# Performance work log

Measured on AMD Instinct MI355X. Metric: run time of the kernel, lower is better.

Reference implementation:

```python
import jax, jax.numpy as jnp
import numpy as np

NUM_HEADS = 4
NUM_GROUPS = 8
EPS = 1e-5


def setup_inputs() -> dict:
    key = jax.random.key(0)
    ks = jax.random.split(key, 4)
    b, c, h, w = 16, 512, 32, 32
    x = jax.random.normal(ks[0], (b, c, h, w), dtype=jnp.float32)
    norm_gamma = jnp.ones((c,), dtype=jnp.float32)
    norm_beta = jnp.zeros((c,), dtype=jnp.float32)
    qkv_w = jax.random.normal(ks[1], (3 * c, c), dtype=jnp.float32) * (c ** -0.5)
    qkv_b = jnp.zeros((3 * c,), dtype=jnp.float32)
    proj_w = jax.random.normal(ks[2], (c, c), dtype=jnp.float32) * (c ** -0.5)
    proj_b = jnp.zeros((c,), dtype=jnp.float32)
    return {"x": x, "norm_gamma": norm_gamma, "norm_beta": norm_beta,
            "qkv_w": qkv_w, "qkv_b": qkv_b, "proj_w": proj_w, "proj_b": proj_b}


def reference(x, norm_gamma, norm_beta, qkv_w, qkv_b, proj_w, proj_b):
    b, c, h, w = x.shape
    nh = NUM_HEADS
    dh = c // nh
    n = h * w
    # GroupNorm(8, c): normalize over (c/G, h, w) within each group, biased var
    xg = x.reshape(b, NUM_GROUPS, -1)
    mu = jnp.mean(xg, axis=-1, keepdims=True)
    var = jnp.var(xg, axis=-1, keepdims=True)
    xn = ((xg - mu) * jax.lax.rsqrt(var + EPS)).reshape(b, c, h, w)
    xn = xn * norm_gamma[:, None, None] + norm_beta[:, None, None]
    # QKV 1x1 conv == channel matmul
    qkv = jnp.einsum('oc,bchw->bohw', qkv_w, xn) + qkv_b[:, None, None]
    q, k, v = jnp.split(qkv, 3, axis=1)  # each [b, c, h, w]

    def to_heads(t):  # [b, c, h, w] -> [b, nh, n, dh]
        return t.reshape(b, nh, dh, n).transpose(0, 1, 3, 2)

    q, k, v = to_heads(q), to_heads(k), to_heads(v)
    scale = dh ** -0.5
    attn = jax.nn.softmax(jnp.einsum('bhnd,bhmd->bhnm', q, k) * scale, axis=-1)
    out = jnp.einsum('bhnm,bhmd->bhnd', attn, v)  # [b, nh, n, dh]
    out = out.transpose(0, 1, 3, 2).reshape(b, c, h, w)
    out = jnp.einsum('oc,bchw->bohw', proj_w, out) + proj_b[:, None, None]
    return x + out
```

## Files before the change

kernel.cpp:

```cpp
#include <hip/hip_runtime.h>

typedef unsigned short u16;
typedef unsigned int   u32;

typedef __attribute__((ext_vector_type(8)))  short bf16x8;
typedef __attribute__((ext_vector_type(16))) float f32x16;
#define MFMA32(a, b, c) __builtin_amdgcn_mfma_f32_32x32x16_bf16(a, b, c, 0, 0, 0)

__device__ __forceinline__ float bf2f(u16 h) { return __uint_as_float(((u32)h) << 16); }
__device__ __forceinline__ u16 f2bf(float f) {
  u32 u = __float_as_uint(f);
  u += 0x7fffu + ((u >> 16) & 1u);
  return (u16)(u >> 16);
}
__device__ __forceinline__ void unpack8(uint4 u, float* f) {
  f[0] = __uint_as_float(u.x << 16); f[1] = __uint_as_float(u.x & 0xffff0000u);
  f[2] = __uint_as_float(u.y << 16); f[3] = __uint_as_float(u.y & 0xffff0000u);
  f[4] = __uint_as_float(u.z << 16); f[5] = __uint_as_float(u.z & 0xffff0000u);
  f[6] = __uint_as_float(u.w << 16); f[7] = __uint_as_float(u.w & 0xffff0000u);
}
__device__ __forceinline__ void unpack4(uint2 u, float* f) {
  f[0] = __uint_as_float(u.x << 16); f[1] = __uint_as_float(u.x & 0xffff0000u);
  f[2] = __uint_as_float(u.y << 16); f[3] = __uint_as_float(u.y & 0xffff0000u);
}

template <bool F>
__device__ __forceinline__ void load8(const void* p, size_t idx, float* f) {
  if constexpr (F) {
    const float4* q = (const float4*)((const float*)p + idx);
    float4 a = q[0], b = q[1];
    f[0] = a.x; f[1] = a.y; f[2] = a.z; f[3] = a.w;
    f[4] = b.x; f[5] = b.y; f[6] = b.z; f[7] = b.w;
  } else {
    unpack8(*(const uint4*)((const u16*)p + idx), f);
  }
}
template <bool F>
__device__ __forceinline__ void load4(const void* p, size_t idx, float* f) {
  if constexpr (F) {
    float4 a = *(const float4*)((const float*)p + idx);
    f[0] = a.x; f[1] = a.y; f[2] = a.z; f[3] = a.w;
  } else {
    unpack4(*(const uint2*)((const u16*)p + idx), f);
  }
}
template <bool F>
__device__ __forceinline__ float load1(const void* p, size_t idx) {
  if constexpr (F) return ((const float*)p)[idx];
  else return bf2f(((const u16*)p)[idx]);
}

__device__ __forceinline__ void gl2lds16(const void* g, void* l) {
  __builtin_amdgcn_global_load_lds(
      (const __attribute__((address_space(1))) void*)g,
      (__attribute__((address_space(3))) void*)l, 16, 0, 0);
}

__global__ void detect_dtype(const void* __restrict__ x, int* __restrict__ flag) {
  if (threadIdx.x == 0 && blockIdx.x == 0) {
    const u32* p = (const u32*)x;
    int sane = 0;
    for (int i = 0; i < 256; ++i) {
      u32 e = (p[i] >> 7) & 0xFFu;
      sane += (e >= 100u && e <= 150u) ? 1 : 0;
    }
    *flag = (sane < 192) ? 1 : 0;
  }
}

__global__ void signal_ws(u16* __restrict__ out, int n) {
  int i = blockIdx.x * 256 + threadIdx.x;
  if (i < n) out[i] = 0x42C8;
}

#define SM_SCALE 0.08838834764831843f
#define QSC 0.12751743f


template <bool F>
__global__ void __launch_bounds__(256) wconv(const void* __restrict__ qkvw,
                                             const void* __restrict__ qkvb,
                                             u16* __restrict__ dst,
                                             const int* __restrict__ flag) {
  if ((flag[0] != 0) != F) return;
  int i = blockIdx.x * 256 + threadIdx.x;
  if (i < 786432) {
    dst[i] = F ? f2bf(((const float*)qkvw)[i]) : ((const u16*)qkvw)[i];
  } else if (i < 787968) {
    int j = i - 786432;
    dst[i] = F ? f2bf(((const float*)qkvb)[j]) : ((const u16*)qkvb)[j];
  }
}

template <bool F>
__global__ void __launch_bounds__(256) gn_norm(const void* __restrict__ x,
                                               const void* __restrict__ gamma,
                                               const void* __restrict__ beta,
                                               u16* __restrict__ xT,
                                               const int* __restrict__ flag) {
  if ((flag[0] != 0) != F) return;
  const int g = blockIdx.x, b = blockIdx.y;
  const int tid = threadIdx.x;
  const size_t base = (size_t)(b * 512 + g * 64) * 1024;
  float sum = 0.f, sq = 0.f;
  for (int i = tid; i < 8192; i += 256) {
    float f[8]; load8<F>(x, base + (size_t)i * 8, f);
#pragma unroll
    for (int m = 0; m < 8; ++m) { sum += f[m]; sq += f[m] * f[m]; }
  }
  __shared__ float ssum[256], ssq[256];
  ssum[tid] = sum; ssq[tid] = sq; __syncthreads();
  for (int off = 128; off > 0; off >>= 1) {
    if (tid < off) { ssum[tid] += ssum[tid + off]; ssq[tid] += ssq[tid + off]; }
    __syncthreads();
  }
  __shared__ float scb[64], bsb[64];
  if (tid < 64) {
    float mu  = ssum[0] * (1.f / 65536.f);
    float var = ssq[0] * (1.f / 65536.f) - mu * mu;
    float s = load1<F>(gamma, g * 64 + tid) * rsqrtf(var + 1e-5f);
    scb[tid] = s;
    bsb[tid] = load1<F>(beta, g * 64 + tid) - mu * s;
  }
  __syncthreads();

  __shared__ float Tf[64][65];
  for (int s0 = 0; s0 < 1024; s0 += 64) {
#pragma unroll
    for (int half = 0; half < 2; ++half) {
      int idx = tid + half * 256;
      int c_loc = idx >> 3, s8 = (idx & 7) * 8;
      float f[8];
      load8<F>(x, base + (size_t)c_loc * 1024 + s0 + s8, f);
      float sm = scb[c_loc], ba = bsb[c_loc];
#pragma unroll
      for (int m = 0; m < 8; ++m) Tf[s8 + m][c_loc] = f[m] * sm + ba;
    }
    __syncthreads();
#pragma unroll
    for (int half = 0; half < 2; ++half) {
      int idx = tid + half * 256;
      int s_loc = idx >> 3, c8 = (idx & 7) * 8;
      u32 pk[4];
#pragma unroll
      for (int m = 0; m < 4; ++m)
        pk[m] = (u32)f2bf(Tf[s_loc][c8 + 2 * m]) |
                ((u32)f2bf(Tf[s_loc][c8 + 2 * m + 1]) << 16);
      *(uint4*)(xT + (size_t)(b * 1024 + s0 + s_loc) * 512 + g * 64 + c8) =
          make_uint4(pk[0], pk[1], pk[2], pk[3]);
    }
    __syncthreads();
  }
}

template <bool QSCALE, bool BIASN>
__global__ void __launch_bounds__(256, 4)
gemm_lds(const u16* __restrict__ A, const u16* __restrict__ B,
         const u16* __restrict__ bias, u16* __restrict__ outp,
         size_t aOff, size_t aBatch, size_t bBatch, int biasOff, size_t oBatch) {
  const int n0 = blockIdx.x * 128;
  const int m0 = blockIdx.y * 128;
  const int b  = blockIdx.z;
  __shared__ __align__(16) u16 At[8192];
  __shared__ __align__(16) u16 Bt[8192];
  const int tid = threadIdx.x;
  const int w = tid >> 6, lane = tid & 63;
  const int lo = lane & 31, hi = lane >> 5;
  const int wm = w >> 1, wn = w & 1;
  const u16* Ab = A + aOff + (size_t)b * aBatch;
  const u16* Bb = B + (size_t)b * bBatch;
  const int srow = lane >> 3, spc = lane & 7;

  f32x16 cA[2][2];
#pragma unroll
  for (int i = 0; i < 2; ++i)
#pragma unroll
    for (int j = 0; j < 2; ++j)
#pragma unroll
      for (int r = 0; r < 16; ++r) cA[i][j][r] = 0.f;

  for (int kt = 0; kt < 8; ++kt) {
    const int kb = kt * 64;
#pragma unroll
    for (int c = 0; c < 4; ++c) {
      int grp = w * 4 + c;
      int row = grp * 8 + srow;
      int lc  = spc ^ (row & 7);
      gl2lds16(Ab + (size_t)(m0 + row) * 512 + kb + lc * 8, &At[grp * 512]);
      gl2lds16(Bb + (size_t)(n0 + row) * 512 + kb + lc * 8, &Bt[grp * 512]);
    }
    __syncthreads();
#pragma unroll
    for (int k16 = 0; k16 < 4; ++k16) {
      const int lc = k16 * 2 + hi;
      const int rA0 = wm * 64 + lo,  rA1 = rA0 + 32;
      const int rB0 = wn * 64 + lo,  rB1 = rB0 + 32;
      bf16x8 a0 = *(const bf16x8*)&At[rA0 * 64 + ((lc ^ (rA0 & 7)) << 3)];
      bf16x8 a1 = *(const bf16x8*)&At[rA1 * 64 + ((lc ^ (rA1 & 7)) << 3)];
      bf16x8 b0 = *(const bf16x8*)&Bt[rB0 * 64 + ((lc ^ (rB0 & 7)) << 3)];
      bf16x8 b1 = *(const bf16x8*)&Bt[rB1 * 64 + ((lc ^ (rB1 & 7)) << 3)];
      cA[0][0] = MFMA32(a0, b0, cA[0][0]);
      cA[0][1] = MFMA32(a0, b1, cA[0][1]);
      cA[1][0] = MFMA32(a1, b0, cA[1][0]);
      cA[1][1] = MFMA32(a1, b1, cA[1][1]);
    }
    __syncthreads();
  }

  float bcol[2];
  if constexpr (BIASN) {
    bcol[0] = bf2f(bias[biasOff + n0 + wn * 64 + lo]);
    bcol[1] = bf2f(bias[biasOff + n0 + wn * 64 + 32 + lo]);
  }
#pragma unroll
  for (int mt = 0; mt < 2; ++mt)
#pragma unroll
    for (int nt = 0; nt < 2; ++nt) {
      const int nbase = n0 + wn * 64 + nt * 32;
      float scl = 1.f;
      if constexpr (QSCALE) scl = (nbase < 512) ? QSC : 1.f;
#pragma unroll
      for (int r = 0; r < 16; ++r) {
        int m = m0 + wm * 64 + mt * 32 + (r & 3) + 8 * (r >> 2) + 4 * hi;
        int n = nbase + lo;
        float v = cA[mt][nt][r];
        if constexpr (BIASN) v += bcol[nt];
        else                 v += bf2f(bias[biasOff + m]);
        if constexpr (QSCALE) v *= scl;
        outp[(size_t)b * oBatch + (size_t)m * 1024 + n] = f2bf(v);
      }
    }
}

template <bool F, bool AEXT, bool BEXT, bool BIASN, bool RESID, bool FOUT>
__global__ void __launch_bounds__(256, 4)
gemm_mfma(const void* __restrict__ A, const void* __restrict__ B,
          const void* __restrict__ bias, const void* __restrict__ resid,
          void* __restrict__ outp,
          size_t aOff, size_t bOff, int biasOff,
          size_t aBatch, size_t bBatch, size_t oBatch, size_t rBatch,
          const int* __restrict__ flag) {
  if ((flag[0] != 0) != F) return;
  const int n0 = blockIdx.x * 128;
  const int m0 = blockIdx.y * 128;
  const int b  = blockIdx.z;
  __shared__ __align__(16) u16 At[128][72];
  __shared__ __align__(16) u16 Bt[128][72];
  const int tid = threadIdx.x;
  const int w = tid >> 6, lane = tid & 63;
  const int lo = lane & 31, hi = lane >> 5;
  const int wm = w >> 1, wn = w & 1;
  const size_t aBase = aOff + (size_t)b * aBatch;
  const size_t bBase = bOff + (size_t)b * bBatch;

  f32x16 cA[2][2];
#pragma unroll
  for (int i = 0; i < 2; ++i)
#pragma unroll
    for (int j = 0; j < 2; ++j)
#pragma unroll
      for (int r = 0; r < 16; ++r) cA[i][j][r] = 0.f;

  for (int kt = 0; kt < 8; ++kt) {
#pragma unroll
    for (int i = 0; i < 4; ++i) {
      int idx = tid + i * 256;
      int row = idx >> 3, kc = (idx & 7) * 8;
      int k = kt * 64 + kc;
      {
        if constexpr (AEXT && F) {
          float f[8]; load8<true>(A, aBase + (size_t)(m0 + row) * 512 + k, f);
          u32 w0 = (u32)f2bf(f[0]) | ((u32)f2bf(f[1]) << 16);
          u32 w1 = (u32)f2bf(f[2]) | ((u32)f2bf(f[3]) << 16);
          u32 w2 = (u32)f2bf(f[4]) | ((u32)f2bf(f[5]) << 16);
          u32 w3 = (u32)f2bf(f[6]) | ((u32)f2bf(f[7]) << 16);
          *(uint4*)&At[row][kc] = make_uint4(w0, w1, w2, w3);
        } else {
          *(uint4*)&At[row][kc] =
              *(const uint4*)((const u16*)A + aBase + (size_t)(m0 + row) * 512 + k);
        }
      }
      {
        if constexpr (BEXT && F) {
          float f[8]; load8<true>(B, bBase + (size_t)(n0 + row) * 512 + k, f);
          u32 w0 = (u32)f2bf(f[0]) | ((u32)f2bf(f[1]) << 16);
          u32 w1 = (u32)f2bf(f[2]) | ((u32)f2bf(f[3]) << 16);
          u32 w2 = (u32)f2bf(f[4]) | ((u32)f2bf(f[5]) << 16);
          u32 w3 = (u32)f2bf(f[6]) | ((u32)f2bf(f[7]) << 16);
          *(uint4*)&Bt[row][kc] = make_uint4(w0, w1, w2, w3);
        } else {
          *(uint4*)&Bt[row][kc] =
              *(const uint4*)((const u16*)B + bBase + (size_t)(n0 + row) * 512 + k);
        }
      }
    }
    __syncthreads();
#pragma unroll
    for (int k16 = 0; k16 < 4; ++k16) {
      const int ko = k16 * 16 + hi * 8;
      bf16x8 a0 = *(const bf16x8*)&At[wm * 64 + lo][ko];
      bf16x8 a1 = *(const bf16x8*)&At[wm * 64 + 32 + lo][ko];
      bf16x8 b0 = *(const bf16x8*)&Bt[wn * 64 + lo][ko];
      bf16x8 b1 = *(const bf16x8*)&Bt[wn * 64 + 32 + lo][ko];
      cA[0][0] = MFMA32(a0, b0, cA[0][0]);
      cA[0][1] = MFMA32(a0, b1, cA[0][1]);
      cA[1][0] = MFMA32(a1, b0, cA[1][0]);
      cA[1][1] = MFMA32(a1, b1, cA[1][1]);
    }
    __syncthreads();
  }

  float bcol[2];
  if constexpr (BIASN) {
    bcol[0] = load1<F>(bias, biasOff + n0 + wn * 64 + lo);
    bcol[1] = load1<F>(bias, biasOff + n0 + wn * 64 + 32 + lo);
  }
#pragma unroll
  for (int mt = 0; mt < 2; ++mt)
#pragma unroll
    for (int nt = 0; nt < 2; ++nt) {
#pragma unroll
      for (int r = 0; r < 16; ++r) {
        int m = m0 + wm * 64 + mt * 32 + (r & 3) + 8 * (r >> 2) + 4 * hi;
        int n = n0 + wn * 64 + nt * 32 + lo;
        float v = cA[mt][nt][r];
        if constexpr (BIASN) v += bcol[nt];
        else                 v += load1<F>(bias, biasOff + m);
        if constexpr (RESID)
          v += load1<F>(resid, (size_t)b * rBatch + (size_t)m * 1024 + n);
        size_t off = (size_t)b * oBatch + (size_t)m * 1024 + n;
        if constexpr (FOUT) ((float*)outp)[off] = v;
        else                ((u16*)outp)[off] = f2bf(v);
      }
    }
}

__global__ void __launch_bounds__(256, 2) attn4(const u16* __restrict__ qkT,
                                                const u16* __restrict__ V,
                                                u16* __restrict__ aout) {
  const int bh = blockIdx.x;
  const int q0 = blockIdx.y * 128;
  const int b = bh >> 2, h = bh & 3;
  const u16* qt = qkT + (size_t)b * 1048576;
  const u16* vb = V + (size_t)b * 524288 + (size_t)(h * 128) * 1024;
  __shared__ __align__(16) u16 smem[25600];
  const int tid = threadIdx.x;
  const int w = tid >> 6, lane = tid & 63;
  const int lo = lane & 31, hi = lane >> 5;

#pragma unroll
  for (int c = 0; c < 8; ++c) {
    int grp = w * 8 + c;
    int row = grp * 4 + (lane >> 4);
    int lc  = (lane & 15) ^ (row & 7);
    gl2lds16(qt + (size_t)(q0 + row) * 1024 + h * 128 + lc * 8, &smem[grp * 512]);
  }
  __syncthreads();
  bf16x8 qf[8];
  {
    const int row = 32 * w + lo;
#pragma unroll
    for (int k16 = 0; k16 < 8; ++k16) {
      int lc = k16 * 2 + hi;
      qf[k16] = *(const bf16x8*)&smem[row * 128 + ((lc ^ (row & 7)) << 3)];
    }
  }

  f32x16 o0, o1, o2, o3;
  float lp[16];
#pragma unroll
  for (int r = 0; r < 16; ++r) { o0[r] = 0.f; o1[r] = 0.f; o2[r] = 0.f; o3[r] = 0.f; lp[r] = 0.f; }

  for (int kt = 0; kt < 16; ++kt) {
    const int k0 = kt * 64;
    __syncthreads();
#pragma unroll
    for (int c = 0; c < 4; ++c) {
      int grp = w * 4 + c;
      {
        int row = grp * 4 + (lane >> 4);
        int lc  = (lane & 15) ^ (row & 7);
        gl2lds16(qt + (size_t)(k0 + row) * 1024 + 512 + h * 128 + lc * 8,
                 &smem[grp * 512]);
      }
      {
        int row = grp * 8 + (lane >> 3);
        int lc  = (lane & 7) ^ (row & 7);
        gl2lds16(vb + (size_t)row * 1024 + k0 + lc * 8, &smem[8192 + grp * 512]);
      }
    }
    __syncthreads();

    f32x16 s0, s1;
#pragma unroll
    for (int r = 0; r < 16; ++r) { s0[r] = 0.f; s1[r] = 0.f; }
#pragma unroll
    for (int k16 = 0; k16 < 8; ++k16) {
      const int lc = k16 * 2 + hi;
      const int r0 = lo, r1 = lo + 32;
      bf16x8 b0 = *(const bf16x8*)&smem[r0 * 128 + ((lc ^ (r0 & 7)) << 3)];
      bf16x8 b1 = *(const bf16x8*)&smem[r1 * 128 + ((lc ^ (r1 & 7)) << 3)];
      s0 = MFMA32(qf[k16], b0, s0);
      s1 = MFMA32(qf[k16], b1, s1);
    }

#pragma unroll
    for (int r = 0; r < 16; ++r) {
      float p0 = exp2f(s0[r]);
      float p1 = exp2f(s1[r]);
      lp[r] += p0 + p1;
      int row = (r & 3) + 8 * (r >> 2) + 4 * hi;
      smem[16384 + w * 2304 + row * 72 + lo]      = f2bf(p0);
      smem[16384 + w * 2304 + row * 72 + lo + 32] = f2bf(p1);
    }

#pragma unroll
    for (int k16v = 0; k16v < 4; ++k16v) {
      bf16x8 pa = *(const bf16x8*)&smem[16384 + w * 2304 + lo * 72 + k16v * 16 + hi * 8];
      const int lc = k16v * 2 + hi;
#pragma unroll
      for (int dt = 0; dt < 4; ++dt) {
        const int row = dt * 32 + lo;
        bf16x8 bv = *(const bf16x8*)&smem[8192 + row * 64 + ((lc ^ (row & 7)) << 3)];
        if (dt == 0) o0 = MFMA32(pa, bv, o0);
        else if (dt == 1) o1 = MFMA32(pa, bv, o1);
        else if (dt == 2) o2 = MFMA32(pa, bv, o2);
        else o3 = MFMA32(pa, bv, o3);
      }
    }
  }

#pragma unroll
  for (int r = 0; r < 16; ++r) {
    float su = lp[r];
    su += __shfl_xor(su, 1);  su += __shfl_xor(su, 2);
    su += __shfl_xor(su, 4);  su += __shfl_xor(su, 8);
    su += __shfl_xor(su, 16);
    float linv = 1.f / su;
    int q = q0 + 32 * w + (r & 3) + 8 * (r >> 2) + 4 * hi;
    size_t base = (size_t)(b * 1024 + q) * 512 + h * 128;
    aout[base +  0 + lo] = f2bf(o0[r] * linv);
    aout[base + 32 + lo] = f2bf(o1[r] * linv);
    aout[base + 64 + lo] = f2bf(o2[r] * linv);
    aout[base + 96 + lo] = f2bf(o3[r] * linv);
  }
}


template <bool F>
__global__ void __launch_bounds__(256) gn_stats(const void* __restrict__ x,
                                                const void* __restrict__ gamma,
                                                const void* __restrict__ beta,
                                                float* __restrict__ sc,
                                                float* __restrict__ bs,
                                                const int* __restrict__ flag) {
  if ((flag[0] != 0) != F) return;
  const int g = blockIdx.x, b = blockIdx.y;
  const int tid = threadIdx.x;
  const size_t base = (size_t)(b * 512 + g * 64) * 1024;
  float sum = 0.f, sq = 0.f;
  for (int i = tid; i < 8192; i += 256) {
    float f[8]; load8<F>(x, base + (size_t)i * 8, f);
#pragma unroll
    for (int m = 0; m < 8; ++m) { sum += f[m]; sq += f[m] * f[m]; }
  }
  __shared__ float ssum[256], ssq[256];
  ssum[tid] = sum; ssq[tid] = sq; __syncthreads();
  for (int off = 128; off > 0; off >>= 1) {
    if (tid < off) { ssum[tid] += ssum[tid + off]; ssq[tid] += ssq[tid + off]; }
    __syncthreads();
  }
  if (tid < 64) {
    float mu  = ssum[0] * (1.f / 65536.f);
    float var = ssq[0] * (1.f / 65536.f) - mu * mu;
    int c = g * 64 + tid;
    float s = load1<F>(gamma, c) * rsqrtf(var + 1e-5f);
    sc[b * 512 + c] = s;
    bs[b * 512 + c] = load1<F>(beta, c) - mu * s;
  }
}

template <bool F, bool BEXT, bool FOUT>
__global__ void __launch_bounds__(256) gemm64(const void* __restrict__ A,
                                              const void* __restrict__ B,
                                              const float* __restrict__ sc,
                                              const float* __restrict__ bs,
                                              const void* __restrict__ bias,
                                              const void* __restrict__ resid,
                                              void* __restrict__ outp,
                                              int mrows, int donorm, int bstride,
                                              const int* __restrict__ flag) {
  if ((flag[0] != 0) != F) return;
  const int s0 = blockIdx.x * 64;
  const int o0 = blockIdx.y * 64;
  const int b  = blockIdx.z;
  __shared__ __align__(16) float At[64][36];
  __shared__ __align__(16) float Bt[64][36];
  const int tid = threadIdx.x;
  const int ty = tid >> 4, tx = tid & 15;
  const int i0 = ty * 4, j0 = tx * 4;
  const int arow = tid >> 2, akc = (tid & 3) * 8;
  const int brow = tid >> 3, bnc = (tid & 7) * 8;
  float acc[4][4] = {};

  for (int kt = 0; kt < 512; kt += 32) {
    float af[8];
    load8<F>(A, (size_t)(o0 + arow) * 512 + akc + kt, af);
    *(float4*)&At[arow][akc]     = make_float4(af[0], af[1], af[2], af[3]);
    *(float4*)&At[arow][akc + 4] = make_float4(af[4], af[5], af[6], af[7]);
    const int c = kt + brow;
    float bf[8];
    load8<(BEXT && F)>(B, (size_t)(b * bstride + c) * 1024 + s0 + bnc, bf);
    float smul = 1.f, badd = 0.f;
    if (donorm) { smul = sc[b * 512 + c]; badd = bs[b * 512 + c]; }
#pragma unroll
    for (int m = 0; m < 8; ++m) Bt[bnc + m][brow] = bf[m] * smul + badd;
    __syncthreads();
#pragma unroll
    for (int kq = 0; kq < 8; ++kq) {
      float4 a0 = *(const float4*)&At[i0 + 0][kq * 4];
      float4 a1 = *(const float4*)&At[i0 + 1][kq * 4];
      float4 a2 = *(const float4*)&At[i0 + 2][kq * 4];
      float4 a3 = *(const float4*)&At[i0 + 3][kq * 4];
      float4 c0 = *(const float4*)&Bt[j0 + 0][kq * 4];
      float4 c1 = *(const float4*)&Bt[j0 + 1][kq * 4];
      float4 c2 = *(const float4*)&Bt[j0 + 2][kq * 4];
      float4 c3 = *(const float4*)&Bt[j0 + 3][kq * 4];
#define DOT4(ii, jj, AV, CV) acc[ii][jj] += AV.x * CV.x + AV.y * CV.y + AV.z * CV.z + AV.w * CV.w;
      DOT4(0,0,a0,c0) DOT4(0,1,a0,c1) DOT4(0,2,a0,c2) DOT4(0,3,a0,c3)
      DOT4(1,0,a1,c0) DOT4(1,1,a1,c1) DOT4(1,2,a1,c2) DOT4(1,3,a1,c3)
      DOT4(2,0,a2,c0) DOT4(2,1,a2,c1) DOT4(2,2,a2,c2) DOT4(2,3,a2,c3)
      DOT4(3,0,a3,c0) DOT4(3,1,a3,c1) DOT4(3,2,a3,c2) DOT4(3,3,a3,c3)
#undef DOT4
    }
    __syncthreads();
  }
#pragma unroll
  for (int ii = 0; ii < 4; ++ii) {
    const int o = o0 + i0 + ii;
    const float bb = load1<F>(bias, o);
    float v[4];
#pragma unroll
    for (int jj = 0; jj < 4; ++jj) v[jj] = acc[ii][jj] + bb;
    if (resid) {
      float xf[4];
      load4<F>(resid, (size_t)(b * 512 + o) * 1024 + s0 + j0, xf);
#pragma unroll
      for (int jj = 0; jj < 4; ++jj) v[jj] += xf[jj];
    }
    const size_t ooff = (size_t)(b * mrows + o) * 1024 + s0 + j0;
    if constexpr (FOUT) {
      *(float4*)((float*)outp + ooff) = make_float4(v[0], v[1], v[2], v[3]);
    } else {
      uint2 pk;
      pk.x = (u32)f2bf(v[0]) | ((u32)f2bf(v[1]) << 16);
      pk.y = (u32)f2bf(v[2]) | ((u32)f2bf(v[3]) << 16);
      *(uint2*)((u16*)outp + ooff) = pk;
    }
  }
}

__global__ void __launch_bounds__(256, 2) attn_old(u16* __restrict__ qkv) {
  const int q0 = blockIdx.x * 128;
  const int bh = blockIdx.y;
  const int b = bh >> 2, h = bh & 3;
  u16* qp = qkv + (size_t)(b * 1536 + h * 128) * 1024;
  const u16* kp = qp + (size_t)512 * 1024;
  const u16* vp = qp + (size_t)1024 * 1024;
  __shared__ __align__(16) u16 Qt[128][136];
  __shared__ __align__(16) u16 Kt[32][136];
  __shared__ __align__(16) u16 Vt[128][40];
  __shared__ __align__(16) u16 Pt[128][40];
  const int tid = threadIdx.x;
  const int w = tid >> 6, lane = tid & 63;
  const int lo = lane & 31, hi = lane >> 5;

  for (int idx = tid; idx < 2048; idx += 256) {
    int d = idx >> 4, s8 = (idx & 15) * 8;
    uint4 qv = *(const uint4*)(qp + (size_t)d * 1024 + q0 + s8);
    const u16* qs = (const u16*)&qv;
#pragma unroll
    for (int m = 0; m < 8; ++m) Qt[s8 + m][d] = qs[m];
  }
  __syncthreads();
  bf16x8 qf[8];
#pragma unroll
  for (int kq = 0; kq < 8; ++kq)
    qf[kq] = *(const bf16x8*)&Qt[32 * w + lo][kq * 16 + hi * 8];

  f32x16 o0, o1, o2, o3;
  float lp[16];
#pragma unroll
  for (int r = 0; r < 16; ++r) { o0[r] = 0.f; o1[r] = 0.f; o2[r] = 0.f; o3[r] = 0.f; lp[r] = 0.f; }

  for (int kt = 0; kt < 32; ++kt) {
    const int k0 = kt * 32;
    __syncthreads();
    for (int idx = tid; idx < 512; idx += 256) {
      int d = idx >> 2, s8 = (idx & 3) * 8;
      uint4 kv = *(const uint4*)(kp + (size_t)d * 1024 + k0 + s8);
      const u16* ks = (const u16*)&kv;
#pragma unroll
      for (int m = 0; m < 8; ++m) Kt[s8 + m][d] = ks[m];
      *(uint4*)&Vt[d][s8] = *(const uint4*)(vp + (size_t)d * 1024 + k0 + s8);
    }
    __syncthreads();
    f32x16 acc;
#pragma unroll
    for (int r = 0; r < 16; ++r) acc[r] = 0.f;
#pragma unroll
    for (int kq = 0; kq < 8; ++kq) {
      bf16x8 bq = *(const bf16x8*)&Kt[lo][kq * 16 + hi * 8];
      acc = MFMA32(qf[kq], bq, acc);
    }
#pragma unroll
    for (int r = 0; r < 16; ++r) {
      float pe = __expf(acc[r] * SM_SCALE);
      lp[r] += pe;
      int row = (r & 3) + 8 * (r >> 2) + 4 * hi;
      Pt[32 * w + row][lo] = f2bf(pe);
    }
    __syncthreads();
#pragma unroll
    for (int kq2 = 0; kq2 < 2; ++kq2) {
      bf16x8 a2 = *(const bf16x8*)&Pt[32 * w + lo][kq2 * 16 + hi * 8];
      bf16x8 b0 = *(const bf16x8*)&Vt[ 0 + lo][kq2 * 16 + hi * 8];
      bf16x8 b1 = *(const bf16x8*)&Vt[32 + lo][kq2 * 16 + hi * 8];
      bf16x8 b2 = *(const bf16x8*)&Vt[64 + lo][kq2 * 16 + hi * 8];
      bf16x8 b3 = *(const bf16x8*)&Vt[96 + lo][kq2 * 16 + hi * 8];
      o0 = MFMA32(a2, b0, o0);
      o1 = MFMA32(a2, b1, o1);
      o2 = MFMA32(a2, b2, o2);
      o3 = MFMA32(a2, b3, o3);
    }
  }
#pragma unroll
  for (int r = 0; r < 16; ++r) {
    float su = lp[r];
    su += __shfl_xor(su, 1);  su += __shfl_xor(su, 2);
    su += __shfl_xor(su, 4);  su += __shfl_xor(su, 8);
    su += __shfl_xor(su, 16);
    float linv = 1.f / su;
    int row = (r & 3) + 8 * (r >> 2) + 4 * hi;
    int q = q0 + 32 * w + row;
    size_t base = (size_t)(b * 1536 + h * 128) * 1024 + q;
    qkv[base + (size_t)( 0 + lo) * 1024] = f2bf(o0[r] * linv);
    qkv[base + (size_t)(32 + lo) * 1024] = f2bf(o1[r] * linv);
    qkv[base + (size_t)(64 + lo) * 1024] = f2bf(o2[r] * linv);
    qkv[base + (size_t)(96 + lo) * 1024] = f2bf(o3[r] * linv);
  }
}

extern "C" void kernel_launch(void* const* d_in, const int* in_sizes, int n_in,
                              void* d_out, int out_size, void* d_ws, size_t ws_size,
                              hipStream_t stream) {
  const void* x     = d_in[0];
  const void* gamma = d_in[1];
  const void* beta  = d_in[2];
  const void* qkvw  = d_in[3];
  const void* qkvb  = d_in[4];
  const void* projw = d_in[5];
  const void* projb = d_in[6];

  char* ws = (char*)d_ws;
  const size_t MB = 1024 * 1024;
  const size_t FAST_NEED = 64 * MB + 64;
  const size_t OLD_NEED  = 48 * MB + 256 + 2 * 16 * 512 * 4;

  if (ws_size >= FAST_NEED) {
    u16* xT   = (u16*)ws;
    u16* qkT  = (u16*)(ws + 16 * MB);
    u16* Vbuf = (u16*)(ws + 48 * MB);
    int* flag = (int*)(ws + 64 * MB);
    u16* wbf  = (u16*)d_out;

    detect_dtype<<<1, 64, 0, stream>>>(x, flag);
    wconv<false><<<3078, 256, 0, stream>>>(qkvw, qkvb, wbf, flag);
    wconv<true ><<<3078, 256, 0, stream>>>(qkvw, qkvb, wbf, flag);
    gn_norm<false><<<dim3(8, 16), 256, 0, stream>>>(x, gamma, beta, xT, flag);
    gn_norm<true ><<<dim3(8, 16), 256, 0, stream>>>(x, gamma, beta, xT, flag);

    gemm_lds<true, true><<<dim3(8, 8, 16), 256, 0, stream>>>(
        xT, wbf, wbf + 786432, qkT, 0, 524288, 0, 0, 1048576);
    gemm_lds<false, false><<<dim3(8, 4, 16), 256, 0, stream>>>(
        wbf, xT, wbf + 786432, Vbuf, 524288, 0, 524288, 1024, 524288);

    attn4<<<dim3(64, 8), 256, 0, stream>>>(qkT, Vbuf, xT);

    gemm_mfma<false, true, false, false, true, false>
        <<<dim3(8, 4, 16), 256, 0, stream>>>(projw, xT, projb, x, d_out,
                                             0, 0, 0, 0, 524288, 524288, 524288, flag);
    gemm_mfma<true, true, false, false, true, true>
        <<<dim3(8, 4, 16), 256, 0, stream>>>(projw, xT, projb, x, d_out,
                                             0, 0, 0, 0, 524288, 524288, 524288, flag);
    return;
  }

  if (ws_size < OLD_NEED) {
    signal_ws<<<(out_size + 255) / 256, 256, 0, stream>>>((u16*)d_out, out_size);
    return;
  }

  const size_t QKV_BYTES = (size_t)16 * 1536 * 1024 * 2;
  u16* qkv  = (u16*)ws;
  int* flag = (int*)(ws + QKV_BYTES);
  float* sc = (float*)(ws + QKV_BYTES + 256);
  float* bs = sc + 16 * 512;

  detect_dtype<<<1, 64, 0, stream>>>(x, flag);
  gn_stats<false><<<dim3(8, 16), 256, 0, stream>>>(x, gamma, beta, sc, bs, flag);
  gn_stats<true ><<<dim3(8, 16), 256, 0, stream>>>(x, gamma, beta, sc, bs, flag);
  gemm64<false, true, false><<<dim3(16, 24, 16), 256, 0, stream>>>(
      qkvw, x, sc, bs, qkvb, nullptr, qkv, 1536, 1, 512, flag);
  gemm64<true, true, false><<<dim3(16, 24, 16), 256, 0, stream>>>(
      qkvw, x, sc, bs, qkvb, nullptr, qkv, 1536, 1, 512, flag);
  attn_old<<<dim3(8, 64), 256, 0, stream>>>(qkv);
  gemm64<false, false, false><<<dim3(16, 8, 16), 256, 0, stream>>>(
      projw, qkv, sc, bs, projb, x, d_out, 512, 0, 1536, flag);
  gemm64<true, false, true><<<dim3(16, 8, 16), 256, 0, stream>>>(
      projw, qkv, sc, bs, projb, x, d_out, 512, 0, 1536, flag);
}
```

Before: 267.3 us.

## Double-buffer K/V tiles and keep attention probabilities in registers

The attention kernel now double-buffers the K and V tiles in shared memory, prefetching the next tile while the current one is computed, which removes one barrier per iteration. It also swaps the QK^T MFMA operands so the score tile is transposed, then packs the probabilities straight into bf16 A-operands with cvt_pk and permlane32_swap instead of sending them through LDS. The row-sum is reduced once at the end with a shuffle broadcast. In exchange, shared memory use per block rises to 64KB, which could limit occupancy, and the code depends on gfx950-specific intrinsics.

```diff
diff --git a/kernel.cpp b/kernel.cpp
--- a/kernel.cpp
+++ b/kernel.cpp
@@ -5,6 +5,7 @@
 
 typedef __attribute__((ext_vector_type(8)))  short bf16x8;
 typedef __attribute__((ext_vector_type(16))) float f32x16;
+typedef __attribute__((ext_vector_type(2)))  unsigned int u32x2;
 #define MFMA32(a, b, c) __builtin_amdgcn_mfma_f32_32x32x16_bf16(a, b, c, 0, 0, 0)
 
 __device__ __forceinline__ float bf2f(u16 h) { return __uint_as_float(((u32)h) << 16); }
@@ -343,7 +344,7 @@
   const int b = bh >> 2, h = bh & 3;
   const u16* qt = qkT + (size_t)b * 1048576;
   const u16* vb = V + (size_t)b * 524288 + (size_t)(h * 128) * 1024;
-  __shared__ __align__(16) u16 smem[25600];
+  __shared__ __align__(16) u16 smem[32768];
   const int tid = threadIdx.x;
   const int w = tid >> 6, lane = tid & 63;
   const int lo = lane & 31, hi = lane >> 5;
@@ -355,6 +356,18 @@
     int lc  = (lane & 15) ^ (row & 7);
     gl2lds16(qt + (size_t)(q0 + row) * 1024 + h * 128 + lc * 8, &smem[grp * 512]);
   }
+#pragma unroll
+  for (int c = 0; c < 4; ++c) {
+    int grp = w * 4 + c;
+    { int row = grp * 4 + (lane >> 4);
+      int lc  = (lane & 15) ^ (row & 7);
+      gl2lds16(qt + (size_t)row * 1024 + 512 + h * 128 + lc * 8,
+               &smem[16384 + grp * 512]); }
+    { int row = grp * 8 + (lane >> 3);
+      int lc  = (lane & 7) ^ (row & 7);
+      gl2lds16(vb + (size_t)row * 1024 + lc * 8,
+               &smem[16384 + 8192 + grp * 512]); }
+  }
   __syncthreads();
   bf16x8 qf[8];
   {
@@ -365,31 +378,34 @@
       qf[k16] = *(const bf16x8*)&smem[row * 128 + ((lc ^ (row & 7)) << 3)];
     }
   }
-
-  f32x16 o0, o1, o2, o3;
-  float lp[16];
-#pragma unroll
-  for (int r = 0; r < 16; ++r) { o0[r] = 0.f; o1[r] = 0.f; o2[r] = 0.f; o3[r] = 0.f; lp[r] = 0.f; }
+  __syncthreads();
+
+  f32x16 o[4];
+  float lp = 0.f;
+#pragma unroll
+  for (int dt = 0; dt < 4; ++dt)
+#pragma unroll
+    for (int r = 0; r < 16; ++r) o[dt][r] = 0.f;
 
   for (int kt = 0; kt < 16; ++kt) {
-    const int k0 = kt * 64;
-    __syncthreads();
-#pragma unroll
-    for (int c = 0; c < 4; ++c) {
-      int grp = w * 4 + c;
-      {
-        int row = grp * 4 + (lane >> 4);
-        int lc  = (lane & 15) ^ (row & 7);
-        gl2lds16(qt + (size_t)(k0 + row) * 1024 + 512 + h * 128 + lc * 8,
-                 &smem[grp * 512]);
+    const u16* rb = &smem[((kt & 1) ^ 1) << 14];
+    u16* wbuf = &smem[(kt & 1) << 14];
+
+    if (kt < 15) {
+      const int k0n = (kt + 1) * 64;
+#pragma unroll
+      for (int c = 0; c < 4; ++c) {
+        int grp = w * 4 + c;
+        { int row = grp * 4 + (lane >> 4);
+          int lc  = (lane & 15) ^ (row & 7);
+          gl2lds16(qt + (size_t)(k0n + row) * 1024 + 512 + h * 128 + lc * 8,
+                   wbuf + grp * 512); }
+        { int row = grp * 8 + (lane >> 3);
+          int lc  = (lane & 7) ^ (row & 7);
+          gl2lds16(vb + (size_t)row * 1024 + k0n + lc * 8,
+                   wbuf + 8192 + grp * 512); }
       }
-      {
-        int row = grp * 8 + (lane >> 3);
-        int lc  = (lane & 7) ^ (row & 7);
-        gl2lds16(vb + (size_t)row * 1024 + k0 + lc * 8, &smem[8192 + grp * 512]);
-      }
-    }
-    __syncthreads();
+    }
 
     f32x16 s0, s1;
 #pragma unroll
@@ -398,51 +414,66 @@
     for (int k16 = 0; k16 < 8; ++k16) {
       const int lc = k16 * 2 + hi;
       const int r0 = lo, r1 = lo + 32;
-      bf16x8 b0 = *(const bf16x8*)&smem[r0 * 128 + ((lc ^ (r0 & 7)) << 3)];
-      bf16x8 b1 = *(const bf16x8*)&smem[r1 * 128 + ((lc ^ (r1 & 7)) << 3)];
-      s0 = MFMA32(qf[k16], b0, s0);
-      s1 = MFMA32(qf[k16], b1, s1);
+      bf16x8 kf0 = *(const bf16x8*)&rb[r0 * 128 + ((lc ^ (r0 & 7)) << 3)];
+      bf16x8 kf1 = *(const bf16x8*)&rb[r1 * 128 + ((lc ^ (r1 & 7)) << 3)];
+      s0 = MFMA32(kf0, qf[k16], s0);
+      s1 = MFMA32(kf1, qf[k16], s1);
     }
 
 #pragma unroll
     for (int r = 0; r < 16; ++r) {
-      float p0 = exp2f(s0[r]);
-      float p1 = exp2f(s1[r]);
-      lp[r] += p0 + p1;
-      int row = (r & 3) + 8 * (r >> 2) + 4 * hi;
-      smem[16384 + w * 2304 + row * 72 + lo]      = f2bf(p0);
-      smem[16384 + w * 2304 + row * 72 + lo + 32] = f2bf(p1);
-    }
-
-#pragma unroll
-    for (int k16v = 0; k16v < 4; ++k16v) {
-      bf16x8 pa = *(const bf16x8*)&smem[16384 + w * 2304 + lo * 72 + k16v * 16 + hi * 8];
-      const int lc = k16v * 2 + hi;
+      s0[r] = exp2f(s0[r]);
+      s1[r] = exp2f(s1[r]);
+      lp += s0[r] + s1[r];
+    }
+
+    bf16x8 pa[4];
+#define MKPA(ps, rb0, dst) do {                                               \
+      u32 qa0, qa1, qb0, qb1;                                                 \
+      asm("v_cvt_pk_bf16_f32 %0, %1, %2" : "=v"(qa0)                          \
+          : "v"((ps)[(rb0) + 0]), "v"((ps)[(rb0) + 1]));                      \
+      asm("v_cvt_pk_bf16_f32 %0, %1, %2" : "=v"(qa1)                          \
+          : "v"((ps)[(rb0) + 2]), "v"((ps)[(rb0) + 3]));                      \
+      asm("v_cvt_pk_bf16_f32 %0, %1, %2" : "=v"(qb0)                          \
+          : "v"((ps)[(rb0) + 4]), "v"((ps)[(rb0) + 5]));                      \
+      asm("v_cvt_pk_bf16_f32 %0, %1, %2" : "=v"(qb1)                          \
+          : "v"((ps)[(rb0) + 6]), "v"((ps)[(rb0) + 7]));                      \
+      u32x2 r0 = __builtin_amdgcn_permlane32_swap(qa0, qb0, false, false);    \
+      u32x2 r1 = __builtin_amdgcn_permlane32_swap(qa1, qb1, false, false);    \
+      union { u32 u[4]; bf16x8 v8; } pk_;                                     \
+      pk_.u[0] = r0[0]; pk_.u[1] = r1[0]; pk_.u[2] = r0[1]; pk_.u[3] = r1[1]; \
+      dst = pk_.v8;                                                           \
+    } while (0)
+    MKPA(s0, 0, pa[0]);
+    MKPA(s0, 8, pa[1]);
+    MKPA(s1, 0, pa[2]);
+    MKPA(s1, 8, pa[3]);
+#undef MKPA
+
+#pragma unroll
+    for (int t = 0; t < 4; ++t) {
+      const int lc = t * 2 + hi;
 #pragma unroll
       for (int dt = 0; dt < 4; ++dt) {
         const int row = dt * 32 + lo;
-        bf16x8 bv = *(const bf16x8*)&smem[8192 + row * 64 + ((lc ^ (row & 7)) << 3)];
-        if (dt == 0) o0 = MFMA32(pa, bv, o0);
-        else if (dt == 1) o1 = MFMA32(pa, bv, o1);
-        else if (dt == 2) o2 = MFMA32(pa, bv, o2);
-        else o3 = MFMA32(pa, bv, o3);
+        bf16x8 bv = *(const bf16x8*)&rb[8192 + row * 64 + ((lc ^ (row & 7)) << 3)];
+        o[dt] = MFMA32(pa[t], bv, o[dt]);
       }
     }
-  }
-
+    __syncthreads();
+  }
+
+  float linv = 1.f / (lp + __shfl_xor(lp, 32));
 #pragma unroll
   for (int r = 0; r < 16; ++r) {
-    float su = lp[r];
-    su += __shfl_xor(su, 1);  su += __shfl_xor(su, 2);
-    su += __shfl_xor(su, 4);  su += __shfl_xor(su, 8);
-    su += __shfl_xor(su, 16);
-    float linv = 1.f / su;
-    int q = q0 + 32 * w + (r & 3) + 8 * (r >> 2) + 4 * hi;
+    int pat = (r & 3) + 8 * (r >> 2) + 4 * hi;
+    float lr = __shfl(linv, pat);
+    int q = q0 + 32 * w + pat;
     size_t base = (size_t)(b * 1024 + q) * 512 + h * 128;
-    aout[base +  0 + lo] = f2bf(o0[r] * linv);
-    aout[base + 32 + lo] = f2bf(o1[r] * linv);
-    aout[base + 64 + lo] = f2bf(o2[r] * linv);
-    aout[base + 96 + lo] = f2bf(o3[r] * linv);
+    aout[base +  0 + lo] = f2bf(o[0][r] * lr);
+    aout[base + 32 + lo] = f2bf(o[1][r] * lr);
+    aout[base + 64 + lo] = f2bf(o[2][r] * lr);
+    aout[base + 96 + lo] = f2bf(o[3][r] * lr);
   }
 }
 
```

After: 257.7 us. -3.6%, faster.
